# Kernel optimization log

Hardware: AMD Instinct MI355X
Metric: run time of the kernel (lower is better)

The kernel has to match this reference:

```python
import jax, jax.numpy as jnp
import numpy as np

B, S, D, H = 1, 4096, 512, 8
HD = D // H  # head_dims = 64


def setup_inputs() -> dict:
    key = jax.random.key(0)
    ks = jax.random.split(key, 12)
    scale = 0.02
    query = jax.random.normal(ks[0], (B, S, D), dtype=jnp.float32)
    key_t = jax.random.normal(ks[1], (B, S, D), dtype=jnp.float32)
    value = jax.random.normal(ks[2], (B, S, D), dtype=jnp.float32)
    mask = jax.random.randint(ks[3], (B, 1, S, S), 0, 2, dtype=jnp.int32)
    # per-head projection params (torch Linear: y = x @ W.T + b)
    Wq = jax.random.normal(ks[4], (HD, HD), dtype=jnp.float32) * scale
    bq = jax.random.normal(ks[5], (HD,), dtype=jnp.float32) * scale
    Wk = jax.random.normal(ks[6], (HD, HD), dtype=jnp.float32) * scale
    bk = jax.random.normal(ks[7], (HD,), dtype=jnp.float32) * scale
    Wv = jax.random.normal(ks[8], (HD, HD), dtype=jnp.float32) * scale
    bv = jax.random.normal(ks[9], (HD,), dtype=jnp.float32) * scale
    Wfc = jax.random.normal(ks[10], (D, D), dtype=jnp.float32) * scale
    bfc = jax.random.normal(ks[11], (D,), dtype=jnp.float32) * scale
    return {"query": query, "key": key_t, "value": value, "mask": mask,
            "Wq": Wq, "bq": bq, "Wk": Wk, "bk": bk, "Wv": Wv, "bv": bv,
            "Wfc": Wfc, "bfc": bfc}


def reference(query, key, value, mask, Wq, bq, Wk, bk, Wv, bv, Wfc, bfc):
    Batch, q_len, _ = query.shape
    k_len = key.shape[1]
    # reshape to [b, s, h, d] then apply per-head linear projections
    q = query.reshape(Batch, q_len, H, HD) @ Wq.T + bq
    k = key.reshape(Batch, k_len, H, HD) @ Wk.T + bk
    v = value.reshape(Batch, k_len, H, HD) @ Wv.T + bv
    # raw scores [b, h, q, k]; mask applied BEFORE scaling (as in original)
    score = jnp.einsum('bqhd,bkhd->bhqk', q, k)
    score = jnp.where(mask == 0, jnp.float32(-1e20), score)
    attn = jax.nn.softmax(score / jnp.sqrt(jnp.float32(HD)), axis=-1)
    out = jnp.einsum('bhqv,bvhd->bqhd', attn, v).reshape(Batch, q_len, D)
    return out @ Wfc.T + bfc
```

## Files before the change

### kernel.cpp

```cpp
#include <hip/hip_runtime.h>
#include <hip/hip_bf16.h>

#define S_LEN 4096
#define DMODEL 512
#define NHEAD 8
#define HDIM 64

typedef __bf16 bf16x8 __attribute__((ext_vector_type(8)));
typedef __bf16 bf16x4 __attribute__((ext_vector_type(4)));
typedef short s16x4 __attribute__((ext_vector_type(4)));
typedef float f32x4 __attribute__((ext_vector_type(4)));

#define S2EXP 0.18033688011112042f

__device__ __forceinline__ void gload_lds16(const void* g, void* l) {
    __builtin_amdgcn_global_load_lds((const __attribute__((address_space(1))) void*)g,
                                     (__attribute__((address_space(3))) void*)l, 16, 0, 0);
}
__device__ __forceinline__ void gload_lds4(const void* g, void* l) {
    __builtin_amdgcn_global_load_lds((const __attribute__((address_space(1))) void*)g,
                                     (__attribute__((address_space(3))) void*)l, 4, 0, 0);
}
__device__ __forceinline__ f32x4 mfma16(bf16x4 a, bf16x4 b, f32x4 c) {
    return __builtin_amdgcn_mfma_f32_16x16x16bf16_1k(__builtin_bit_cast(s16x4, a),
                                                     __builtin_bit_cast(s16x4, b), c, 0, 0, 0);
}

__global__ __launch_bounds__(256) void proj_all_kernel(const float* __restrict__ xq,
                                                       const float* __restrict__ xk,
                                                       const float* __restrict__ xv,
                                                       const float* __restrict__ Wq,
                                                       const float* __restrict__ bq,
                                                       const float* __restrict__ Wk,
                                                       const float* __restrict__ bk,
                                                       const float* __restrict__ Wv,
                                                       const float* __restrict__ bv,
                                                       __bf16* __restrict__ yq,
                                                       __bf16* __restrict__ yk,
                                                       __bf16* __restrict__ vt) {
    __shared__ float T[64][65];
    int bid = blockIdx.x;
    int t = threadIdx.x, wave = t >> 6, lane = t & 63, lg = lane >> 4, lc = lane & 15;
    if (bid < 512) {
        int r0 = bid * 64 + wave * 16;
        const float* xrq = xq + (size_t)(r0 + lc) * 64 + lg * 8;
        const float* xrk = xk + (size_t)(r0 + lc) * 64 + lg * 8;
        bf16x8 aq[2], ak[2];
#pragma unroll
        for (int c = 0; c < 2; ++c) {
            f32x4 u0 = *(const f32x4*)(xrq + c * 32);
            f32x4 u1 = *(const f32x4*)(xrq + c * 32 + 4);
            f32x4 v0 = *(const f32x4*)(xrk + c * 32);
            f32x4 v1 = *(const f32x4*)(xrk + c * 32 + 4);
            bf16x8 a, b;
#pragma unroll
            for (int j = 0; j < 4; ++j) {
                a[j] = (__bf16)u0[j]; a[4 + j] = (__bf16)u1[j];
                b[j] = (__bf16)v0[j]; b[4 + j] = (__bf16)v1[j];
            }
            aq[c] = a; ak[c] = b;
        }
#pragma unroll
        for (int nt = 0; nt < 4; ++nt) {
            const float* wq = Wq + (size_t)(nt * 16 + lc) * 64 + lg * 8;
            const float* wk = Wk + (size_t)(nt * 16 + lc) * 64 + lg * 8;
            f32x4 cq = {0, 0, 0, 0}, ck = {0, 0, 0, 0};
#pragma unroll
            for (int c = 0; c < 2; ++c) {
                f32x4 u0 = *(const f32x4*)(wq + c * 32);
                f32x4 u1 = *(const f32x4*)(wq + c * 32 + 4);
                f32x4 v0 = *(const f32x4*)(wk + c * 32);
                f32x4 v1 = *(const f32x4*)(wk + c * 32 + 4);
                bf16x8 bw, bw2;
#pragma unroll
                for (int j = 0; j < 4; ++j) {
                    bw[j] = (__bf16)u0[j]; bw[4 + j] = (__bf16)u1[j];
                    bw2[j] = (__bf16)v0[j]; bw2[4 + j] = (__bf16)v1[j];
                }
                cq = __builtin_amdgcn_mfma_f32_16x16x32_bf16(aq[c], bw, cq, 0, 0, 0);
                ck = __builtin_amdgcn_mfma_f32_16x16x32_bf16(ak[c], bw2, ck, 0, 0, 0);
            }
            float bqv = bq[nt * 16 + lc], bkv = bk[nt * 16 + lc];
#pragma unroll
            for (int r = 0; r < 4; ++r) {
                yq[(size_t)(r0 + lg * 4 + r) * 64 + nt * 16 + lc] = (__bf16)((cq[r] + bqv) * S2EXP);
                yk[(size_t)(r0 + lg * 4 + r) * 64 + nt * 16 + lc] = (__bf16)(ck[r] + bkv);
            }
        }
    } else {
        int vb = bid - 512;
        int h = vb & 7, s0 = (vb >> 3) * 64;
        const float* xr = xv + ((size_t)(s0 + wave * 16 + lc) * 8 + h) * 64 + lg * 8;
        bf16x8 av[2];
#pragma unroll
        for (int c = 0; c < 2; ++c) {
            f32x4 u0 = *(const f32x4*)(xr + c * 32);
            f32x4 u1 = *(const f32x4*)(xr + c * 32 + 4);
            bf16x8 a;
#pragma unroll
            for (int j = 0; j < 4; ++j) { a[j] = (__bf16)u0[j]; a[4 + j] = (__bf16)u1[j]; }
            av[c] = a;
        }
#pragma unroll
        for (int nt = 0; nt < 4; ++nt) {
            const float* wv = Wv + (size_t)(nt * 16 + lc) * 64 + lg * 8;
            f32x4 cv = {0, 0, 0, 0};
#pragma unroll
            for (int c = 0; c < 2; ++c) {
                f32x4 u0 = *(const f32x4*)(wv + c * 32);
                f32x4 u1 = *(const f32x4*)(wv + c * 32 + 4);
                bf16x8 bw;
#pragma unroll
                for (int j = 0; j < 4; ++j) { bw[j] = (__bf16)u0[j]; bw[4 + j] = (__bf16)u1[j]; }
                cv = __builtin_amdgcn_mfma_f32_16x16x32_bf16(av[c], bw, cv, 0, 0, 0);
            }
            float bvv = bv[nt * 16 + lc];
#pragma unroll
            for (int r = 0; r < 4; ++r) T[wave * 16 + lg * 4 + r][nt * 16 + lc] = cv[r] + bvv;
        }
        __syncthreads();
        int d = t >> 2, qr = t & 3;
        bf16x8 w0, w1;
#pragma unroll
        for (int i = 0; i < 8; ++i) {
            w0[i] = (__bf16)T[qr * 16 + i][d];
            w1[i] = (__bf16)T[qr * 16 + 8 + i][d];
        }
        __bf16* dst = vt + ((size_t)h * 64 + d) * 4096 + s0 + qr * 16;
        *(bf16x8*)(dst) = w0;
        *(bf16x8*)(dst + 8) = w1;
    }
}

__global__ __launch_bounds__(256) void prep_kernel(const int* __restrict__ mask,
                                                   unsigned int* __restrict__ pack,
                                                   const float* __restrict__ Wfc,
                                                   __bf16* __restrict__ wfc_bf) {
    int bid = blockIdx.x;
    int t = threadIdx.x;
    if (bid < 2048) {
        int lane = t & 63;
        int wid = bid * 4 + (t >> 6);
#pragma unroll 4
        for (int it = 0; it < 32; ++it) {
            int gw = wid * 32 + it;
            int qi = gw >> 6, seg = gw & 63;
            unsigned long long bits = __ballot(mask[(size_t)qi * 4096 + seg * 64 + lane] != 0);
            if (lane == 0)
                *(unsigned long long*)(&pack[(size_t)qi * 128 + seg * 2]) = bits;
        }
    } else {
        int b = bid - 2048;
        const f32x4* s4 = (const f32x4*)Wfc;
#pragma unroll
        for (int i = 0; i < 8; ++i) {
            int idx = (b * 8 + i) * 256 + t;
            f32x4 v = s4[idx];
            bf16x4 o;
#pragma unroll
            for (int j = 0; j < 4; ++j) o[j] = (__bf16)v[j];
            *(bf16x4*)(wfc_bf + (size_t)idx * 4) = o;
        }
    }
}

__global__ __launch_bounds__(256, 4) void attn_kernel(const __bf16* __restrict__ qb,
                                                      const __bf16* __restrict__ kb,
                                                      const __bf16* __restrict__ vt,
                                                      const unsigned int* __restrict__ mp,
                                                      int split_steps,
                                                      float* __restrict__ opart,
                                                      float* __restrict__ stats,
                                                      __bf16* __restrict__ ao) {
    int bid = blockIdx.x;
    int h = bid & 7, qtb = (bid >> 3) & 31, sp = bid >> 8;
    int kv0 = sp * split_steps * 32;
    int nsteps = min(split_steps, 128 - sp * split_steps);
    int t = threadIdx.x, wave = t >> 6, lane = t & 63, lg = lane >> 4, lc = lane & 15;
    int q0 = qtb * 128 + wave * 32;

    __shared__ __bf16 Kt[4][32 * 64];
    __shared__ __bf16 Vt[4][64 * 32];
    __shared__ unsigned int Mld[4][128];

    int srK = lane >> 3;
    int cgK = (lane & 7) ^ srK;
    int cgV = ((lane & 3) - ((lane >> 3) & 3)) & 3;
    int srV = lane >> 2;

    const __bf16* qr0 = qb + ((size_t)(q0 + lc) * 8 + h) * 64 + lg * 8;
    const __bf16* qr1 = qb + ((size_t)(q0 + 16 + lc) * 8 + h) * 64 + lg * 8;
    bf16x8 qf00 = *(const bf16x8*)(qr0);
    bf16x8 qf01 = *(const bf16x8*)(qr0 + 32);
    bf16x8 qf10 = *(const bf16x8*)(qr1);
    bf16x8 qf11 = *(const bf16x8*)(qr1 + 32);

    bf16x4 onesA;
#pragma unroll
    for (int j = 0; j < 4; ++j) onesA[j] = (__bf16)1.0f;

    f32x4 o00 = {0,0,0,0}, o01 = {0,0,0,0}, o02 = {0,0,0,0}, o03 = {0,0,0,0};
    f32x4 o10 = {0,0,0,0}, o11 = {0,0,0,0}, o12 = {0,0,0,0}, o13 = {0,0,0,0};
    f32x4 lac0 = {0,0,0,0}, lac1 = {0,0,0,0};

    const __bf16* vbase = vt + (size_t)h * 64 * 4096;
    const unsigned int* mbase = mp + (size_t)(qtb * 128 + wave * 64 + lane) * 128 + (kv0 >> 5);

    int lg4 = lg * 4;
    int vch0 = ((((lg >> 1) + (lc >> 1)) & 3) * 16) + (lg & 1) * 8;
    int vch1 = (((2 + (lg >> 1) + (lc >> 1)) & 3) * 16) + (lg & 1) * 8;

#define STAGE(tt, B)                                                                          \
    {                                                                                         \
        if (wave < 2) gload_lds4(mbase + (tt), &Mld[B][wave * 64]);                           \
        gload_lds16(kb + (size_t)(kv0 + (tt) * 32 + wave * 8 + srK) * 512 + h * 64 + cgK * 8, \
                    &Kt[B][wave * 512]);                                                      \
        gload_lds16(vbase + (size_t)(wave * 16 + srV) * 4096 + kv0 + (tt) * 32 + cgV * 8,     \
                    &Vt[B][wave * 512]);                                                      \
    }

    STAGE(0, 0)
    STAGE(1, 1)
    asm volatile("s_waitcnt vmcnt(0)" ::: "memory");
    __builtin_amdgcn_s_barrier();

#define ATTN_STEP(s, C, G)                                                                    \
    {                                                                                         \
        STAGE(min((s) + 2, nsteps - 1), G)                                                    \
        asm volatile("s_waitcnt vmcnt(4)" ::: "memory");                                      \
        __builtin_amdgcn_s_barrier();                                                         \
        unsigned int mw0 = Mld[C][wave * 32 + lc] >> lg4;                                     \
        unsigned int mw1 = Mld[C][wave * 32 + 16 + lc] >> lg4;                                \
        const char* Kb = (const char*)&Kt[C][0];                                              \
        f32x4 s00 = {0,0,0,0}, s01 = {0,0,0,0}, s10 = {0,0,0,0}, s11 = {0,0,0,0};             \
        {                                                                                     \
            int row = lc, sw = (row & 7) << 4;                                                \
            bf16x8 ka = *(const bf16x8*)(Kb + ((row * 128 + lg * 16) ^ sw));                  \
            bf16x8 kc_ = *(const bf16x8*)(Kb + ((row * 128 + 64 + lg * 16) ^ sw));            \
            __builtin_amdgcn_s_setprio(1);                                                    \
            s00 = __builtin_amdgcn_mfma_f32_16x16x32_bf16(ka, qf00, s00, 0, 0, 0);            \
            s00 = __builtin_amdgcn_mfma_f32_16x16x32_bf16(kc_, qf01, s00, 0, 0, 0);           \
            s01 = __builtin_amdgcn_mfma_f32_16x16x32_bf16(ka, qf10, s01, 0, 0, 0);            \
            s01 = __builtin_amdgcn_mfma_f32_16x16x32_bf16(kc_, qf11, s01, 0, 0, 0);           \
            __builtin_amdgcn_s_setprio(0);                                                    \
        }                                                                                     \
        {                                                                                     \
            int row = 16 + lc, sw = (row & 7) << 4;                                           \
            bf16x8 ka = *(const bf16x8*)(Kb + ((row * 128 + lg * 16) ^ sw));                  \
            bf16x8 kc_ = *(const bf16x8*)(Kb + ((row * 128 + 64 + lg * 16) ^ sw));            \
            __builtin_amdgcn_s_setprio(1);                                                    \
            s10 = __builtin_amdgcn_mfma_f32_16x16x32_bf16(ka, qf00, s10, 0, 0, 0);            \
            s10 = __builtin_amdgcn_mfma_f32_16x16x32_bf16(kc_, qf01, s10, 0, 0, 0);           \
            s11 = __builtin_amdgcn_mfma_f32_16x16x32_bf16(ka, qf10, s11, 0, 0, 0);            \
            s11 = __builtin_amdgcn_mfma_f32_16x16x32_bf16(kc_, qf11, s11, 0, 0, 0);           \
            __builtin_amdgcn_s_setprio(0);                                                    \
        }                                                                                     \
        bf16x4 pk00, pk10, pk01, pk11;                                        \
        _Pragma("unroll")                                                                     \
        for (int r = 0; r < 4; ++r) {                                                         \
            float pa = __builtin_amdgcn_exp2f(s00[r]);                                        \
            pk00[r] = (__bf16)__int_as_float(__float_as_int(pa) &                             \
                                             __builtin_amdgcn_sbfe((int)mw0, r, 1));          \
            float pc = __builtin_amdgcn_exp2f(s10[r]);                                        \
            pk10[r] = (__bf16)__int_as_float(__float_as_int(pc) &                             \
                                             __builtin_amdgcn_sbfe((int)mw0, 16 + r, 1));     \
            float pd = __builtin_amdgcn_exp2f(s01[r]);                                        \
            pk01[r] = (__bf16)__int_as_float(__float_as_int(pd) &                             \
                                             __builtin_amdgcn_sbfe((int)mw1, r, 1));          \
            float pe = __builtin_amdgcn_exp2f(s11[r]);                                        \
            pk11[r] = (__bf16)__int_as_float(__float_as_int(pe) &                             \
                                             __builtin_amdgcn_sbfe((int)mw1, 16 + r, 1));     \
        }                                                                                     \
        const char* Vb = (const char*)&Vt[C][0];                                              \
        bf16x4 v00 = *(const bf16x4*)(Vb + (0 * 16 + lc) * 64 + vch0);                        \
        bf16x4 v01 = *(const bf16x4*)(Vb + (0 * 16 + lc) * 64 + vch1);                        \
        bf16x4 v10 = *(const bf16x4*)(Vb + (1 * 16 + lc) * 64 + vch0);                        \
        bf16x4 v11 = *(const bf16x4*)(Vb + (1 * 16 + lc) * 64 + vch1);                        \
        bf16x4 v20 = *(const bf16x4*)(Vb + (2 * 16 + lc) * 64 + vch0);                        \
        bf16x4 v21 = *(const bf16x4*)(Vb + (2 * 16 + lc) * 64 + vch1);                        \
        bf16x4 v30 = *(const bf16x4*)(Vb + (3 * 16 + lc) * 64 + vch0);                        \
        bf16x4 v31 = *(const bf16x4*)(Vb + (3 * 16 + lc) * 64 + vch1);                        \
        __builtin_amdgcn_s_setprio(1);                                                        \
        lac0 = mfma16(onesA, pk00, lac0);                                                     \
        lac0 = mfma16(onesA, pk10, lac0);                                                     \
        lac1 = mfma16(onesA, pk01, lac1);                                                     \
        lac1 = mfma16(onesA, pk11, lac1);                                                     \
        o00 = mfma16(v00, pk00, o00); o00 = mfma16(v01, pk10, o00);                           \
        o10 = mfma16(v00, pk01, o10); o10 = mfma16(v01, pk11, o10);                           \
        o01 = mfma16(v10, pk00, o01); o01 = mfma16(v11, pk10, o01);                           \
        o11 = mfma16(v10, pk01, o11); o11 = mfma16(v11, pk11, o11);                           \
        o02 = mfma16(v20, pk00, o02); o02 = mfma16(v21, pk10, o02);                           \
        o12 = mfma16(v20, pk01, o12); o12 = mfma16(v21, pk11, o12);                           \
        o03 = mfma16(v30, pk00, o03); o03 = mfma16(v31, pk10, o03);                           \
        o13 = mfma16(v30, pk01, o13); o13 = mfma16(v31, pk11, o13);                           \
        __builtin_amdgcn_s_setprio(0);                                                        \
    }

    for (int s = 0; s < nsteps; s += 4) {
        ATTN_STEP(s + 0, 0, 2)
        ATTN_STEP(s + 1, 1, 3)
        ATTN_STEP(s + 2, 2, 0)
        ATTN_STEP(s + 3, 3, 1)
    }
#undef ATTN_STEP
#undef STAGE

    if (opart) {
        if (lg == 0) {
            stats[(size_t)sp * 32768 + (size_t)(q0 + lc) * 8 + h]      = lac0[0];
            stats[(size_t)sp * 32768 + (size_t)(q0 + 16 + lc) * 8 + h] = lac1[0];
        }
        size_t rh0 = (size_t)sp * 32768 + (size_t)(q0 + lc) * 8 + h;
        size_t rh1 = (size_t)sp * 32768 + (size_t)(q0 + 16 + lc) * 8 + h;
        float* d0 = opart + rh0 * 64 + lg4;
        float* d1 = opart + rh1 * 64 + lg4;
        *(f32x4*)(d0 + 0)  = o00; *(f32x4*)(d0 + 16) = o01;
        *(f32x4*)(d0 + 32) = o02; *(f32x4*)(d0 + 48) = o03;
        *(f32x4*)(d1 + 0)  = o10; *(f32x4*)(d1 + 16) = o11;
        *(f32x4*)(d1 + 32) = o12; *(f32x4*)(d1 + 48) = o13;
    } else {
        float inv0 = 1.0f / lac0[0];
        float inv1 = 1.0f / lac1[0];
        __bf16* d0 = ao + (size_t)(q0 + lc) * 512 + h * 64 + lg4;
        __bf16* d1 = ao + (size_t)(q0 + 16 + lc) * 512 + h * 64 + lg4;
        bf16x4 w;
#pragma unroll
        for (int r = 0; r < 4; ++r) w[r] = (__bf16)(o00[r] * inv0);
        *(bf16x4*)(d0 + 0) = w;
#pragma unroll
        for (int r = 0; r < 4; ++r) w[r] = (__bf16)(o01[r] * inv0);
        *(bf16x4*)(d0 + 16) = w;
#pragma unroll
        for (int r = 0; r < 4; ++r) w[r] = (__bf16)(o02[r] * inv0);
        *(bf16x4*)(d0 + 32) = w;
#pragma unroll
        for (int r = 0; r < 4; ++r) w[r] = (__bf16)(o03[r] * inv0);
        *(bf16x4*)(d0 + 48) = w;
#pragma unroll
        for (int r = 0; r < 4; ++r) w[r] = (__bf16)(o10[r] * inv1);
        *(bf16x4*)(d1 + 0) = w;
#pragma unroll
        for (int r = 0; r < 4; ++r) w[r] = (__bf16)(o11[r] * inv1);
        *(bf16x4*)(d1 + 16) = w;
#pragma unroll
        for (int r = 0; r < 4; ++r) w[r] = (__bf16)(o12[r] * inv1);
        *(bf16x4*)(d1 + 32) = w;
#pragma unroll
        for (int r = 0; r < 4; ++r) w[r] = (__bf16)(o13[r] * inv1);
        *(bf16x4*)(d1 + 48) = w;
    }
}

__global__ __launch_bounds__(256) void combine_kernel(const float* __restrict__ opart,
                                                      const float* __restrict__ stats,
                                                      __bf16* __restrict__ ao, int nsplit) {
    int t = threadIdx.x, lane = t & 63, w = t >> 6;
    int rh = blockIdx.x * 4 + w;
    float L = 0.f, acc = 0.f;
#pragma unroll 3
    for (int sp = 0; sp < nsplit; ++sp) {
        L += stats[(size_t)sp * 32768 + rh];
        acc += opart[((size_t)sp * 32768 + rh) * 64 + lane];
    }
    int row = rh >> 3, h = rh & 7;
    ao[(size_t)row * 512 + h * 64 + lane] = (__bf16)(acc / L);
}

__global__ __launch_bounds__(256) void fc_kernel(const __bf16* __restrict__ ao,
                                                 const __bf16* __restrict__ Wb,
                                                 const float* __restrict__ bfc,
                                                 float* __restrict__ out) {
    int bid = blockIdx.x;
    int stile = bid >> 3, nt = bid & 7;
    int t = threadIdx.x, wave = t >> 6, lane = t & 63, lg = lane >> 4, lc = lane & 15;
    int s0 = stile * 64 + wave * 16;
    int n0 = nt * 64;
    f32x4 c0 = {0,0,0,0}, c1 = {0,0,0,0}, c2 = {0,0,0,0}, c3 = {0,0,0,0};
    for (int k0 = 0; k0 < 512; k0 += 32) {
        bf16x8 af = *(const bf16x8*)(ao + (size_t)(s0 + lc) * 512 + k0 + lg * 8);
        const __bf16* wb = Wb + k0 + lg * 8;
        c0 = __builtin_amdgcn_mfma_f32_16x16x32_bf16(af, *(const bf16x8*)(wb + (size_t)(n0 + 0 * 16 + lc) * 512), c0, 0, 0, 0);
        c1 = __builtin_amdgcn_mfma_f32_16x16x32_bf16(af, *(const bf16x8*)(wb + (size_t)(n0 + 1 * 16 + lc) * 512), c1, 0, 0, 0);
        c2 = __builtin_amdgcn_mfma_f32_16x16x32_bf16(af, *(const bf16x8*)(wb + (size_t)(n0 + 2 * 16 + lc) * 512), c2, 0, 0, 0);
        c3 = __builtin_amdgcn_mfma_f32_16x16x32_bf16(af, *(const bf16x8*)(wb + (size_t)(n0 + 3 * 16 + lc) * 512), c3, 0, 0, 0);
    }
#pragma unroll
    for (int r = 0; r < 4; ++r) {
        int row = s0 + lg * 4 + r;
        float* dst = out + (size_t)row * 512 + n0;
        dst[0 * 16 + lc] = c0[r] + bfc[n0 + 0 * 16 + lc];
        dst[1 * 16 + lc] = c1[r] + bfc[n0 + 1 * 16 + lc];
        dst[2 * 16 + lc] = c2[r] + bfc[n0 + 2 * 16 + lc];
        dst[3 * 16 + lc] = c3[r] + bfc[n0 + 3 * 16 + lc];
    }
}

extern "C" void kernel_launch(void* const* d_in, const int* in_sizes, int n_in,
                              void* d_out, int out_size, void* d_ws, size_t ws_size,
                              hipStream_t stream) {
    const float* query = (const float*)d_in[0];
    const float* key   = (const float*)d_in[1];
    const float* value = (const float*)d_in[2];
    const int*   mask  = (const int*)d_in[3];
    const float* Wq  = (const float*)d_in[4];
    const float* bq  = (const float*)d_in[5];
    const float* Wk  = (const float*)d_in[6];
    const float* bk  = (const float*)d_in[7];
    const float* Wv  = (const float*)d_in[8];
    const float* bv  = (const float*)d_in[9];
    const float* Wfc = (const float*)d_in[10];
    const float* bfc = (const float*)d_in[11];

    char* ws = (char*)d_ws;
    const size_t MB = 1024 * 1024;
    __bf16* q_bf   = (__bf16*)(ws + 0 * MB);
    __bf16* k_bf   = (__bf16*)(ws + 4 * MB);
    __bf16* vt     = (__bf16*)(ws + 8 * MB);
    __bf16* ao     = (__bf16*)(ws + 12 * MB);
    __bf16* wfc_bf = (__bf16*)(ws + 16 * MB);
    unsigned int* mpack = (unsigned int*)(ws + 17 * MB);
    const size_t base = 19 * MB;
    int nsplit = (ws_size >= base + 3 * (8 * MB) + 3 * 131072) ? 3 : 1;
    float* opart = (float*)(ws + base);
    float* stats = (float*)(ws + base + (size_t)nsplit * 8 * MB);

    proj_all_kernel<<<1024, 256, 0, stream>>>(query, key, value, Wq, bq, Wk, bk, Wv, bv,
                                              q_bf, k_bf, vt);
    prep_kernel<<<2080, 256, 0, stream>>>(mask, mpack, Wfc, wfc_bf);
    if (nsplit > 1) {
        attn_kernel<<<256 * nsplit, 256, 0, stream>>>(q_bf, k_bf, vt, mpack,
                                                      44, opart, stats, ao);
        combine_kernel<<<8192, 256, 0, stream>>>(opart, stats, ao, nsplit);
    } else {
        attn_kernel<<<256, 256, 0, stream>>>(q_bf, k_bf, vt, mpack,
                                             128, nullptr, nullptr, ao);
    }
    fc_kernel<<<512, 256, 0, stream>>>(ao, wfc_bf, bfc, (float*)d_out);
}
```

Baseline: 120.1 us.

## Fuse split-K combine into FC GEMM and merge projection with mask-pack prep

Merges the projection kernel and the mask-pack/Wfc-convert kernel into one launch. Folds the split-softmax combine step into the output FC kernel, which reads the three partial outputs and stats directly, normalizes them and converts to bf16 as the A operand. This removes two kernel launches and the intermediate ao round trip through memory. In exchange, each FC block rereads the fp32 partials (three times the data) once per column tile, so opart traffic grows eightfold. The split count of three is also hardcoded in the fused path.

```diff
diff --git a/kernel.cpp b/kernel.cpp
--- a/kernel.cpp
+++ b/kernel.cpp
@@ -12,6 +12,7 @@
 typedef float f32x4 __attribute__((ext_vector_type(4)));
 
 #define S2EXP 0.18033688011112042f
+#define OPSTRIDE 2097152
 
 __device__ __forceinline__ void gload_lds16(const void* g, void* l) {
     __builtin_amdgcn_global_load_lds((const __attribute__((address_space(1))) void*)g,
@@ -26,18 +27,22 @@
                                                      __builtin_bit_cast(s16x4, b), c, 0, 0, 0);
 }
 
-__global__ __launch_bounds__(256) void proj_all_kernel(const float* __restrict__ xq,
-                                                       const float* __restrict__ xk,
-                                                       const float* __restrict__ xv,
-                                                       const float* __restrict__ Wq,
-                                                       const float* __restrict__ bq,
-                                                       const float* __restrict__ Wk,
-                                                       const float* __restrict__ bk,
-                                                       const float* __restrict__ Wv,
-                                                       const float* __restrict__ bv,
-                                                       __bf16* __restrict__ yq,
-                                                       __bf16* __restrict__ yk,
-                                                       __bf16* __restrict__ vt) {
+__global__ __launch_bounds__(256) void pre_kernel(const float* __restrict__ xq,
+                                                  const float* __restrict__ xk,
+                                                  const float* __restrict__ xv,
+                                                  const float* __restrict__ Wq,
+                                                  const float* __restrict__ bq,
+                                                  const float* __restrict__ Wk,
+                                                  const float* __restrict__ bk,
+                                                  const float* __restrict__ Wv,
+                                                  const float* __restrict__ bv,
+                                                  __bf16* __restrict__ yq,
+                                                  __bf16* __restrict__ yk,
+                                                  __bf16* __restrict__ vt,
+                                                  const int* __restrict__ mask,
+                                                  unsigned int* __restrict__ pack,
+                                                  const float* __restrict__ Wfc,
+                                                  __bf16* __restrict__ wfc_bf) {
     __shared__ float T[64][65];
     int bid = blockIdx.x;
     int t = threadIdx.x, wave = t >> 6, lane = t & 63, lg = lane >> 4, lc = lane & 15;
@@ -87,7 +92,7 @@
                 yk[(size_t)(r0 + lg * 4 + r) * 64 + nt * 16 + lc] = (__bf16)(ck[r] + bkv);
             }
         }
-    } else {
+    } else if (bid < 1024) {
         int vb = bid - 512;
         int h = vb & 7, s0 = (vb >> 3) * 64;
         const float* xr = xv + ((size_t)(s0 + wave * 16 + lc) * 8 + h) * 64 + lg * 8;
@@ -129,18 +134,8 @@
         __bf16* dst = vt + ((size_t)h * 64 + d) * 4096 + s0 + qr * 16;
         *(bf16x8*)(dst) = w0;
         *(bf16x8*)(dst + 8) = w1;
-    }
-}
-
-__global__ __launch_bounds__(256) void prep_kernel(const int* __restrict__ mask,
-                                                   unsigned int* __restrict__ pack,
-                                                   const float* __restrict__ Wfc,
-                                                   __bf16* __restrict__ wfc_bf) {
-    int bid = blockIdx.x;
-    int t = threadIdx.x;
-    if (bid < 2048) {
-        int lane = t & 63;
-        int wid = bid * 4 + (t >> 6);
+    } else if (bid < 3072) {
+        int wid = (bid - 1024) * 4 + (t >> 6);
 #pragma unroll 4
         for (int it = 0; it < 32; ++it) {
             int gw = wid * 32 + it;
@@ -150,7 +145,7 @@
                 *(unsigned long long*)(&pack[(size_t)qi * 128 + seg * 2]) = bits;
         }
     } else {
-        int b = bid - 2048;
+        int b = bid - 3072;
         const f32x4* s4 = (const f32x4*)Wfc;
 #pragma unroll
         for (int i = 0; i < 8; ++i) {
@@ -255,7 +250,7 @@
             s11 = __builtin_amdgcn_mfma_f32_16x16x32_bf16(kc_, qf11, s11, 0, 0, 0);           \
             __builtin_amdgcn_s_setprio(0);                                                    \
         }                                                                                     \
-        bf16x4 pk00, pk10, pk01, pk11;                                        \
+        bf16x4 pk00, pk10, pk01, pk11;                                                        \
         _Pragma("unroll")                                                                     \
         for (int r = 0; r < 4; ++r) {                                                         \
             float pa = __builtin_amdgcn_exp2f(s00[r]);                                        \
@@ -351,19 +346,54 @@
     }
 }
 
-__global__ __launch_bounds__(256) void combine_kernel(const float* __restrict__ opart,
-                                                      const float* __restrict__ stats,
-                                                      __bf16* __restrict__ ao, int nsplit) {
-    int t = threadIdx.x, lane = t & 63, w = t >> 6;
-    int rh = blockIdx.x * 4 + w;
-    float L = 0.f, acc = 0.f;
-#pragma unroll 3
-    for (int sp = 0; sp < nsplit; ++sp) {
-        L += stats[(size_t)sp * 32768 + rh];
-        acc += opart[((size_t)sp * 32768 + rh) * 64 + lane];
-    }
-    int row = rh >> 3, h = rh & 7;
-    ao[(size_t)row * 512 + h * 64 + lane] = (__bf16)(acc / L);
+__global__ __launch_bounds__(256) void fc_fused_kernel(const float* __restrict__ opart,
+                                                       const float* __restrict__ stats,
+                                                       const __bf16* __restrict__ Wb,
+                                                       const float* __restrict__ bfc,
+                                                       float* __restrict__ out) {
+    int bid = blockIdx.x;
+    int stile = bid >> 3, nt = bid & 7;
+    int t = threadIdx.x, wave = t >> 6, lane = t & 63, lg = lane >> 4, lc = lane & 15;
+    int s0 = stile * 64 + wave * 16;
+    int n0 = nt * 64;
+    f32x4 c0 = {0,0,0,0}, c1 = {0,0,0,0}, c2 = {0,0,0,0}, c3 = {0,0,0,0};
+    for (int h2 = 0; h2 < 8; ++h2) {
+        size_t rh = (size_t)(s0 + lc) * 8 + h2;
+        float L = stats[rh] + stats[32768 + rh] + stats[65536 + rh];
+        float inv = 1.0f / L;
+        const float* ob = opart + rh * 64;
+#pragma unroll
+        for (int half = 0; half < 2; ++half) {
+            int d0 = half * 32 + lg * 8;
+            f32x4 a0 = *(const f32x4*)(ob + d0);
+            f32x4 a1 = *(const f32x4*)(ob + d0 + 4);
+            f32x4 b0 = *(const f32x4*)(ob + OPSTRIDE + d0);
+            f32x4 b1 = *(const f32x4*)(ob + OPSTRIDE + d0 + 4);
+            f32x4 e0 = *(const f32x4*)(ob + 2 * OPSTRIDE + d0);
+            f32x4 e1 = *(const f32x4*)(ob + 2 * OPSTRIDE + d0 + 4);
+            bf16x8 af;
+#pragma unroll
+            for (int j = 0; j < 4; ++j) {
+                af[j]     = (__bf16)((a0[j] + b0[j] + e0[j]) * inv);
+                af[4 + j] = (__bf16)((a1[j] + b1[j] + e1[j]) * inv);
+            }
+            int k0 = h2 * 64 + half * 32;
+            const __bf16* wb = Wb + k0 + lg * 8;
+            c0 = __builtin_amdgcn_mfma_f32_16x16x32_bf16(af, *(const bf16x8*)(wb + (size_t)(n0 + 0 * 16 + lc) * 512), c0, 0, 0, 0);
+            c1 = __builtin_amdgcn_mfma_f32_16x16x32_bf16(af, *(const bf16x8*)(wb + (size_t)(n0 + 1 * 16 + lc) * 512), c1, 0, 0, 0);
+            c2 = __builtin_amdgcn_mfma_f32_16x16x32_bf16(af, *(const bf16x8*)(wb + (size_t)(n0 + 2 * 16 + lc) * 512), c2, 0, 0, 0);
+            c3 = __builtin_amdgcn_mfma_f32_16x16x32_bf16(af, *(const bf16x8*)(wb + (size_t)(n0 + 3 * 16 + lc) * 512), c3, 0, 0, 0);
+        }
+    }
+#pragma unroll
+    for (int r = 0; r < 4; ++r) {
+        int row = s0 + lg * 4 + r;
+        float* dst = out + (size_t)row * 512 + n0;
+        dst[0 * 16 + lc] = c0[r] + bfc[n0 + 0 * 16 + lc];
+        dst[1 * 16 + lc] = c1[r] + bfc[n0 + 1 * 16 + lc];
+        dst[2 * 16 + lc] = c2[r] + bfc[n0 + 2 * 16 + lc];
+        dst[3 * 16 + lc] = c3[r] + bfc[n0 + 3 * 16 + lc];
+    }
 }
 
 __global__ __launch_bounds__(256) void fc_kernel(const __bf16* __restrict__ ao,
@@ -424,16 +454,15 @@
     float* opart = (float*)(ws + base);
     float* stats = (float*)(ws + base + (size_t)nsplit * 8 * MB);
 
-    proj_all_kernel<<<1024, 256, 0, stream>>>(query, key, value, Wq, bq, Wk, bk, Wv, bv,
-                                              q_bf, k_bf, vt);
-    prep_kernel<<<2080, 256, 0, stream>>>(mask, mpack, Wfc, wfc_bf);
+    pre_kernel<<<3104, 256, 0, stream>>>(query, key, value, Wq, bq, Wk, bk, Wv, bv,
+                                         q_bf, k_bf, vt, mask, mpack, Wfc, wfc_bf);
     if (nsplit > 1) {
         attn_kernel<<<256 * nsplit, 256, 0, stream>>>(q_bf, k_bf, vt, mpack,
                                                       44, opart, stats, ao);
-        combine_kernel<<<8192, 256, 0, stream>>>(opart, stats, ao, nsplit);
+        fc_fused_kernel<<<512, 256, 0, stream>>>(opart, stats, wfc_bf, bfc, (float*)d_out);
     } else {
         attn_kernel<<<256, 256, 0, stream>>>(q_bf, k_bf, vt, mpack,
                                              128, nullptr, nullptr, ao);
-    }
-    fc_kernel<<<512, 256, 0, stream>>>(ao, wfc_bf, bfc, (float*)d_out);
-}
+        fc_kernel<<<512, 256, 0, stream>>>(ao, wfc_bf, bfc, (float*)d_out);
+    }
+}
```

Measured after the change: 143.1 us. 19.2% more time.
